# Kernel tuning notes

Hardware: AMD Instinct MI355X
Metric: run time of the kernel (lower is better)

## Reference

```python
import jax, jax.numpy as jnp
import numpy as np

DIM = 100      # number of assets in the basket
M = 50         # time steps
T = 1.0
R = 0.05
SIGMA = 0.2
S0 = 100.0
DT = T / M
H = 128        # hidden_dim of ZetaNetwork
B = 8192       # Monte-Carlo paths (batch)
EPS = 1e-5     # torch LayerNorm eps


def _layernorm(x, g, b):
    mu = jnp.mean(x, axis=-1, keepdims=True)
    var = jnp.mean((x - mu) ** 2, axis=-1, keepdims=True)
    return (x - mu) / jnp.sqrt(var + EPS) * g + b


def setup_inputs() -> dict:
    key = jax.random.key(0)
    ks = jax.random.split(key, 12)
    dw = jax.random.normal(ks[0], (B, M, DIM), dtype=jnp.float32)
    t_grid = jax.random.uniform(ks[1], (B, M), dtype=jnp.float32)
    s = 0.05
    inp = {
        "dw": dw,
        "t_grid": t_grid,
        "W1": jax.random.normal(ks[2], (DIM + 1, H), dtype=jnp.float32) * s,
        "b1": jnp.zeros((H,), jnp.float32),
        "g1": jnp.ones((H,), jnp.float32),
        "be1": jnp.zeros((H,), jnp.float32),
        "W2": jax.random.normal(ks[3], (H, H), dtype=jnp.float32) * s,
        "b2": jnp.zeros((H,), jnp.float32),
        "g2": jnp.ones((H,), jnp.float32),
        "be2": jnp.zeros((H,), jnp.float32),
        "W3": jax.random.normal(ks[4], (H, H), dtype=jnp.float32) * s,
        "b3": jnp.zeros((H,), jnp.float32),
        "g3": jnp.ones((H,), jnp.float32),
        "be3": jnp.zeros((H,), jnp.float32),
        "W4": jax.random.normal(ks[5], (H, DIM), dtype=jnp.float32) * s,
        "b4": jnp.zeros((DIM,), jnp.float32),
        "Y0": jnp.array([10.0], dtype=jnp.float32),
    }
    return inp


def reference(dw, t_grid, W1, b1, g1, be1, W2, b2, g2, be2,
              W3, b3, g3, be3, W4, b4, Y0):
    batch = dw.shape[0]

    def zeta_net(x):  # x: [B, DIM+1]
        h = jax.nn.gelu(_layernorm(x @ W1 + b1, g1, be1), approximate=False)
        h = jax.nn.gelu(_layernorm(h @ W2 + b2, g2, be2), approximate=False)
        h = jax.nn.gelu(_layernorm(h @ W3 + b3, g3, be3), approximate=False)
        return jax.nn.sigmoid(h @ W4 + b4)  # [B, DIM]

    def step(carry, xs):
        S, Y = carry
        dw_i, t_i = xs                                   # [B,DIM], [B,1]
        net_in = jnp.concatenate([S / S0, t_i], axis=1)  # [B,DIM+1]
        zeta = zeta_net(net_in)
        dS = S * (R * DT + SIGMA * dw_i)
        portfolio_gain = jnp.sum(zeta * dS, axis=1, keepdims=True)
        asset_val = jnp.sum(zeta * S, axis=1, keepdims=True)
        Y = Y + R * (Y - asset_val) * DT + portfolio_gain
        S = S + dS
        return (S, Y), None

    S_init = jnp.full((batch, DIM), S0, dtype=dw.dtype)
    Y_init = jnp.ones((batch, 1), dtype=dw.dtype) * Y0
    xs = (jnp.swapaxes(dw, 0, 1),                # [M,B,DIM]
          jnp.swapaxes(t_grid, 0, 1)[..., None])  # [M,B,1]
    (S, Y), _ = jax.lax.scan(step, (S_init, Y_init), xs)
    return (Y, S)
```

## Files before the change

### kernel.cpp

```cpp
#include <hip/hip_runtime.h>
#include <hip/hip_bf16.h>
#include <cstdint>
#include <cstddef>

typedef __attribute__((ext_vector_type(8))) short short8;
typedef __attribute__((ext_vector_type(4))) float f32x4;
typedef __attribute__((ext_vector_type(4))) unsigned int u32x4;

#define NDIM 100
#define NSTEP 50
#define NPATH 8192
#define XSTR 128
#define ESTR 128

typedef const __attribute__((address_space(1))) unsigned int glb_u32;
typedef __attribute__((address_space(3))) unsigned int lds_u32;

__device__ __forceinline__ unsigned short f2b(float f){
  unsigned int u = __float_as_uint(f);
  u += 0x7fffu + ((u >> 16) & 1u);
  return (unsigned short)(u >> 16);
}
__device__ __forceinline__ float b2f(unsigned short h){
  return __uint_as_float(((unsigned int)h) << 16);
}
__device__ __forceinline__ float gelu_fast(float y){
  float u = __builtin_amdgcn_exp2f(-2.4554673f * y);
  return y * __builtin_amdgcn_rcpf(1.f + u);
}
__device__ __forceinline__ float sigm_fast(float x){
  float u = __builtin_amdgcn_exp2f(-1.4426950f * x);
  return __builtin_amdgcn_rcpf(1.f + u);
}

__global__ __launch_bounds__(256) void prep_weights(
    const float* __restrict__ W1, const float* __restrict__ W2,
    const float* __restrict__ W3, const float* __restrict__ W4,
    unsigned short* __restrict__ WTS)
{
  int idx = blockIdx.x * 256 + threadIdx.x;
  int j = idx & 7;
  int s = (idx >> 3) & 15;
  int n = (idx >> 7) & 127;
  int L = idx >> 14;
  int lc = s ^ (n & 15);
  int k  = j * 16 + lc;
  float v;
  if (L == 0)      v = (k <= NDIM) ? W1[k * 128 + n] : 0.f;
  else if (L == 1) v = W2[k * 128 + n];
  else if (L == 2) v = W3[k * 128 + n];
  else             v = (n < NDIM) ? W4[k * NDIM + n] : 0.f;
  WTS[idx] = f2b(v);
}

__global__ __launch_bounds__(256) void prep_params(
    const float* __restrict__ b1, const float* __restrict__ g1, const float* __restrict__ be1,
    const float* __restrict__ b2, const float* __restrict__ g2, const float* __restrict__ be2,
    const float* __restrict__ b3, const float* __restrict__ g3, const float* __restrict__ be3,
    const float* __restrict__ b4, float* __restrict__ PPAR)
{
  int idx = blockIdx.x * 256 + threadIdx.x;
  if (idx >= 1536) return;
  int ct = idx & 7;
  int c  = (idx >> 3) & 15;
  int p  = (idx >> 7) % 3;
  int L  = idx / 384;
  int col = ct * 16 + c;
  const float* v;
  if (L == 0)      v = (p == 0) ? b1 : (p == 1) ? g1 : be1;
  else if (L == 1) v = (p == 0) ? b2 : (p == 1) ? g2 : be2;
  else if (L == 2) v = (p == 0) ? b3 : (p == 1) ? g3 : be3;
  else             v = b4;
  float val;
  if (L == 3) val = (p == 0 && col < NDIM) ? b4[col] : 0.f;
  else        val = v[col];
  PPAR[idx] = val;
}

__global__ __launch_bounds__(256) void phaseA(
    const float* __restrict__ dw, const float* __restrict__ tg,
    unsigned short* __restrict__ X, unsigned short* __restrict__ E,
    float* __restrict__ Sout, int path0)
{
  const int pb = threadIdx.x >> 6;
  const int t  = threadIdx.x & 63;
  const int bl = blockIdx.x * 4 + pb;
  const int b  = path0 + bl;
  const int d0 = (t & 7) * 16 + (t >> 3);
  const int d1 = d0 + 8;
  float s0 = 100.f, s1 = 100.f;
  const float* dwb = dw + (long)b * NSTEP * NDIM;
  const float* tgb = tg + (long)b * NSTEP;
  unsigned short* Xb = X + (long)bl * NSTEP * XSTR;
  unsigned short* Eb = E + (long)bl * NSTEP * ESTR;
  for (int i = 0; i < NSTEP; ++i){
    float tv = tgb[i];
    float w0 = (d0 < NDIM) ? dwb[i * NDIM + d0] : 0.f;
    float w1 = (d1 < NDIM) ? dwb[i * NDIM + d1] : 0.f;
    unsigned short* Xr = Xb + i * XSTR;
    unsigned short* Er = Eb + i * ESTR;
    Xr[t]      = (d0 < NDIM) ? f2b(s0 * 0.01f) : ((d0 == NDIM) ? f2b(tv) : (unsigned short)0);
    Xr[t + 64] = (d1 < NDIM) ? f2b(s1 * 0.01f) : (unsigned short)0;
    Er[t]      = (d0 < NDIM) ? f2b(0.2f * s0 * w0) : (unsigned short)0;
    Er[t + 64] = (d1 < NDIM) ? f2b(0.2f * s1 * w1) : (unsigned short)0;
    s0 = fmaf(s0, 0.001f + 0.2f * w0, s0);
    s1 = fmaf(s1, 0.001f + 0.2f * w1, s1);
  }
  if (d0 < NDIM) Sout[(long)b * NDIM + d0] = s0;
  if (d1 < NDIM) Sout[(long)b * NDIM + d1] = s1;
}

__global__ __launch_bounds__(256, 3) void phaseB(
    const unsigned short* __restrict__ X,
    const unsigned short* __restrict__ E,
    const unsigned short* __restrict__ WTS,
    const float* __restrict__ PPAR,
    float* __restrict__ cbuf, long row0)
{
  __shared__ __align__(16) char lds[49152];
  char* const wbuf = lds;
  const int tid = threadIdx.x;
  const int w = tid >> 6;
  const int l = tid & 63;
  const int g = l >> 4;
  const int c = l & 15;
  char* const H = lds + 32768 + w * 4096;
  const long base = (long)blockIdx.x * 128 + w * 16;

  auto stage = [&](int Loff){
    #pragma unroll
    for (int it = 0; it < 8; ++it){
      int chunk = w * 8 + it;
      __builtin_amdgcn_global_load_lds((glb_u32*)(WTS + Loff + chunk * 512 + l * 8),
          (lds_u32*)(wbuf + chunk * 1024), 16, 0, 0);
    }
  };

  short8 af0[4], af1[4];
  {
    const unsigned short* xr0 = X + (base + c) * XSTR;
    const unsigned short* xr1 = X + (base + 64 + c) * XSTR;
    #pragma unroll
    for (int ks = 0; ks < 4; ++ks){
      af0[ks] = *(const short8*)(xr0 + 32 * ks + 8 * g);
      af1[ks] = *(const short8*)(xr1 + 32 * ks + 8 * g);
    }
  }

  auto mfma2 = [&](f32x4 (&acc0)[8], f32x4 (&acc1)[8], f32x4 blo, f32x4 bhi){
    #pragma unroll
    for (int ct = 0; ct < 8; ++ct){
      float bs = (ct < 4) ? blo[ct] : bhi[ct - 4];
      f32x4 z; z[0] = bs; z[1] = bs; z[2] = bs; z[3] = bs;
      acc0[ct] = z; acc1[ct] = z;
      const char* rowp = wbuf + ((ct * 16 + c) << 8);
      #pragma unroll
      for (int ks = 0; ks < 4; ++ks){
        short8 bf = *(const short8*)(rowp + (((4 * ks + g) ^ c) << 4));
        acc0[ct] = __builtin_amdgcn_mfma_f32_16x16x32_bf16(af0[ks], bf, acc0[ct], 0, 0, 0);
        acc1[ct] = __builtin_amdgcn_mfma_f32_16x16x32_bf16(af1[ks], bf, acc1[ct], 0, 0, 0);
      }
    }
  };

  auto postproc = [&](f32x4 (&acc)[8], short8 (&af)[4],
                      f32x4 glo, f32x4 ghi, f32x4 belo, f32x4 behi){
    #pragma unroll
    for (int j = 0; j < 4; ++j){
      float s1 = 0.f, s2 = 0.f;
      #pragma unroll
      for (int ct = 0; ct < 8; ++ct){ float x = acc[ct][j]; s1 += x; s2 = fmaf(x, x, s2); }
      s1 += __shfl_xor(s1, 1, 64); s2 += __shfl_xor(s2, 1, 64);
      s1 += __shfl_xor(s1, 2, 64); s2 += __shfl_xor(s2, 2, 64);
      s1 += __shfl_xor(s1, 4, 64); s2 += __shfl_xor(s2, 4, 64);
      s1 += __shfl_xor(s1, 8, 64); s2 += __shfl_xor(s2, 8, 64);
      float mu = s1 * 0.0078125f;
      float rstd = rsqrtf(fmaf(-mu, mu, s2 * 0.0078125f) + 1e-5f);
      int row = 4 * g + j;
      u32x4 ov;
      #pragma unroll
      for (int p = 0; p < 4; ++p){
        float ga  = (p < 2) ? glo[2*p]     : ghi[2*p - 4];
        float gb  = (p < 2) ? glo[2*p + 1] : ghi[2*p - 3];
        float ba  = (p < 2) ? belo[2*p]     : behi[2*p - 4];
        float bb2 = (p < 2) ? belo[2*p + 1] : behi[2*p - 3];
        float A0 = rstd * ga, A1 = rstd * gb;
        float C0 = fmaf(-mu, A0, ba), C1 = fmaf(-mu, A1, bb2);
        float h0 = gelu_fast(fmaf(acc[2*p    ][j], A0, C0));
        float h1 = gelu_fast(fmaf(acc[2*p + 1][j], A1, C1));
        unsigned int pk;
        asm("v_cvt_pk_bf16_f32 %0, %1, %2" : "=v"(pk) : "v"(h0), "v"(h1));
        ov[p] = pk;
      }
      *(u32x4*)(H + row * 256 + ((c ^ row) << 4)) = ov;
    }
    #pragma unroll
    for (int ks = 0; ks < 4; ++ks)
      af[ks] = *(const short8*)(H + c * 256 + (((4 * ks + g) ^ c) << 4));
  };

  auto epilogue = [&](f32x4 (&acc)[8], short8 (&ep)[4], long rbase){
    #pragma unroll
    for (int j = 0; j < 4; ++j){
      float pg = 0.f;
      #pragma unroll
      for (int ct = 0; ct < 8; ++ct){
        float z = sigm_fast(acc[ct][j]);
        pg = fmaf(z, b2f((unsigned short)ep[j][ct]), pg);
      }
      pg += __shfl_xor(pg, 1, 64);
      pg += __shfl_xor(pg, 2, 64);
      pg += __shfl_xor(pg, 4, 64);
      pg += __shfl_xor(pg, 8, 64);
      if (c == 0) cbuf[row0 + rbase + 4 * g + j] = pg;
    }
  };

  stage(0);
  __syncthreads();

  #pragma unroll
  for (int L = 0; L < 3; ++L){
    const float* pp = PPAR + L * 384 + c * 8;
    f32x4 blo  = *(const f32x4*)pp,         bhi  = *(const f32x4*)(pp + 4);
    f32x4 glo  = *(const f32x4*)(pp + 128), ghi  = *(const f32x4*)(pp + 132);
    f32x4 belo = *(const f32x4*)(pp + 256), behi = *(const f32x4*)(pp + 260);
    f32x4 acc0[8], acc1[8];
    mfma2(acc0, acc1, blo, bhi);
    __syncthreads();
    stage((L + 1) * 16384);
    postproc(acc0, af0, glo, ghi, belo, behi);
    postproc(acc1, af1, glo, ghi, belo, behi);
    __syncthreads();
  }

  {
    const float* pp = PPAR + 3 * 384 + c * 8;
    f32x4 blo = *(const f32x4*)pp, bhi = *(const f32x4*)(pp + 4);
    short8 ep0[4], ep1[4];
    #pragma unroll
    for (int j = 0; j < 4; ++j){
      ep0[j] = *(const short8*)(E + (base + 4 * g + j) * ESTR + c * 8);
      ep1[j] = *(const short8*)(E + (base + 64 + 4 * g + j) * ESTR + c * 8);
    }
    f32x4 acc0[8], acc1[8];
    mfma2(acc0, acc1, blo, bhi);
    epilogue(acc0, ep0, base);
    epilogue(acc1, ep1, base + 64);
  }
}

__global__ __launch_bounds__(256) void phaseC(const float* __restrict__ cbuf,
                                              const float* __restrict__ Y0,
                                              float* __restrict__ Yout)
{
  int b = blockIdx.x * 256 + threadIdx.x;
  if (b >= NPATH) return;
  const float kk = 1.0f + 0.05f * (1.0f / 50.0f);
  float y = Y0[0];
  const float* cb = cbuf + (long)b * NSTEP;
  #pragma unroll 10
  for (int i = 0; i < NSTEP; ++i) y = y * kk + cb[i];
  Yout[b] = y;
}

extern "C" void kernel_launch(void* const* d_in, const int* in_sizes, int n_in,
                              void* d_out, int out_size, void* d_ws, size_t ws_size,
                              hipStream_t stream)
{
  const float* dw  = (const float*)d_in[0];
  const float* tg  = (const float*)d_in[1];
  const float* W1  = (const float*)d_in[2];
  const float* b1  = (const float*)d_in[3];
  const float* g1  = (const float*)d_in[4];
  const float* be1 = (const float*)d_in[5];
  const float* W2  = (const float*)d_in[6];
  const float* b2  = (const float*)d_in[7];
  const float* g2  = (const float*)d_in[8];
  const float* be2 = (const float*)d_in[9];
  const float* W3  = (const float*)d_in[10];
  const float* b3  = (const float*)d_in[11];
  const float* g3  = (const float*)d_in[12];
  const float* be3 = (const float*)d_in[13];
  const float* W4  = (const float*)d_in[14];
  const float* b4  = (const float*)d_in[15];
  const float* Y0  = (const float*)d_in[16];
  float* out = (float*)d_out;

  char* ws = (char*)d_ws;
  unsigned short* WTS = (unsigned short*)ws;
  float* PPAR = (float*)(ws + 131072);
  float* cbuf = (float*)(ws + 137344);
  char* chunk = ws + 1775744;

  prep_weights<<<256, 256, 0, stream>>>(W1, W2, W3, W4, WTS);
  prep_params<<<6, 256, 0, stream>>>(b1, g1, be1, b2, g2, be2, b3, g3, be3, b4, PPAR);

  long avail = (long)ws_size - 1775744L;
  long pc = (avail > 0) ? (avail / 25600L) : 0;
  if (pc > 8192) pc = 8192;
  pc -= pc % 128;
  if (pc < 128) pc = 128;

  for (long p0 = 0; p0 < 8192; p0 += pc){
    long np = 8192 - p0; if (np > pc) np = pc;
    unsigned short* Xc = (unsigned short*)chunk;
    unsigned short* Ec = Xc + np * 50L * XSTR;
    phaseA<<<(int)(np / 4), 256, 0, stream>>>(dw, tg, Xc, Ec, out + 8192, (int)p0);
    long nrows = np * 50L;
    phaseB<<<(int)(nrows / 128), 256, 0, stream>>>(Xc, Ec, WTS, PPAR, cbuf, p0 * 50L);
  }
  phaseC<<<32, 256, 0, stream>>>(cbuf, Y0, out);
}
```

Before: 215.5 us.

## Double phaseB block to 512 threads and pack LayerNorm/GELU math into float2

phaseB now runs 8 waves per block covering 256 rows instead of 128. Each 32KB weight stage into LDS is therefore shared by twice as many rows, and staging work per wave is halved. The LayerNorm statistics, GELU and sigmoid epilogue are rewritten over float2 pairs so the compiler can emit packed FP32 instructions, and the gamma/beta loads are moved after the MFMA block. LDS per block grows to 64KB, which limits how many blocks fit per CU and may change latency hiding.

```diff
diff --git a/kernel.cpp b/kernel.cpp
--- a/kernel.cpp
+++ b/kernel.cpp
@@ -5,6 +5,7 @@
 
 typedef __attribute__((ext_vector_type(8))) short short8;
 typedef __attribute__((ext_vector_type(4))) float f32x4;
+typedef __attribute__((ext_vector_type(2))) float f32x2;
 typedef __attribute__((ext_vector_type(4))) unsigned int u32x4;
 
 #define NDIM 100
@@ -23,14 +24,6 @@
 }
 __device__ __forceinline__ float b2f(unsigned short h){
   return __uint_as_float(((unsigned int)h) << 16);
-}
-__device__ __forceinline__ float gelu_fast(float y){
-  float u = __builtin_amdgcn_exp2f(-2.4554673f * y);
-  return y * __builtin_amdgcn_rcpf(1.f + u);
-}
-__device__ __forceinline__ float sigm_fast(float x){
-  float u = __builtin_amdgcn_exp2f(-1.4426950f * x);
-  return __builtin_amdgcn_rcpf(1.f + u);
 }
 
 __global__ __launch_bounds__(256) void prep_weights(
@@ -110,14 +103,14 @@
   if (d1 < NDIM) Sout[(long)b * NDIM + d1] = s1;
 }
 
-__global__ __launch_bounds__(256, 3) void phaseB(
+__global__ __launch_bounds__(512, 4) void phaseB(
     const unsigned short* __restrict__ X,
     const unsigned short* __restrict__ E,
     const unsigned short* __restrict__ WTS,
     const float* __restrict__ PPAR,
     float* __restrict__ cbuf, long row0)
 {
-  __shared__ __align__(16) char lds[49152];
+  __shared__ __align__(16) char lds[65536];
   char* const wbuf = lds;
   const int tid = threadIdx.x;
   const int w = tid >> 6;
@@ -125,12 +118,12 @@
   const int g = l >> 4;
   const int c = l & 15;
   char* const H = lds + 32768 + w * 4096;
-  const long base = (long)blockIdx.x * 128 + w * 16;
+  const long base = (long)blockIdx.x * 256 + w * 16;
 
   auto stage = [&](int Loff){
     #pragma unroll
-    for (int it = 0; it < 8; ++it){
-      int chunk = w * 8 + it;
+    for (int it = 0; it < 4; ++it){
+      int chunk = it * 8 + w;
       __builtin_amdgcn_global_load_lds((glb_u32*)(WTS + Loff + chunk * 512 + l * 8),
           (lds_u32*)(wbuf + chunk * 1024), 16, 0, 0);
     }
@@ -139,7 +132,7 @@
   short8 af0[4], af1[4];
   {
     const unsigned short* xr0 = X + (base + c) * XSTR;
-    const unsigned short* xr1 = X + (base + 64 + c) * XSTR;
+    const unsigned short* xr1 = X + (base + 128 + c) * XSTR;
     #pragma unroll
     for (int ks = 0; ks < 4; ++ks){
       af0[ks] = *(const short8*)(xr0 + 32 * ks + 8 * g);
@@ -163,56 +156,106 @@
     }
   };
 
+  auto gelu2 = [&](f32x2 y) -> f32x2 {
+    f32x2 a = y * -2.4554673f;
+    f32x2 u;
+    u[0] = __builtin_amdgcn_exp2f(a[0]);
+    u[1] = __builtin_amdgcn_exp2f(a[1]);
+    f32x2 d = u + 1.0f;
+    f32x2 r;
+    r[0] = __builtin_amdgcn_rcpf(d[0]);
+    r[1] = __builtin_amdgcn_rcpf(d[1]);
+    return y * r;
+  };
+
   auto postproc = [&](f32x4 (&acc)[8], short8 (&af)[4],
                       f32x4 glo, f32x4 ghi, f32x4 belo, f32x4 behi){
-    #pragma unroll
-    for (int j = 0; j < 4; ++j){
-      float s1 = 0.f, s2 = 0.f;
-      #pragma unroll
-      for (int ct = 0; ct < 8; ++ct){ float x = acc[ct][j]; s1 += x; s2 = fmaf(x, x, s2); }
-      s1 += __shfl_xor(s1, 1, 64); s2 += __shfl_xor(s2, 1, 64);
-      s1 += __shfl_xor(s1, 2, 64); s2 += __shfl_xor(s2, 2, 64);
-      s1 += __shfl_xor(s1, 4, 64); s2 += __shfl_xor(s2, 4, 64);
-      s1 += __shfl_xor(s1, 8, 64); s2 += __shfl_xor(s2, 8, 64);
-      float mu = s1 * 0.0078125f;
-      float rstd = rsqrtf(fmaf(-mu, mu, s2 * 0.0078125f) + 1e-5f);
-      int row = 4 * g + j;
-      u32x4 ov;
-      #pragma unroll
-      for (int p = 0; p < 4; ++p){
-        float ga  = (p < 2) ? glo[2*p]     : ghi[2*p - 4];
-        float gb  = (p < 2) ? glo[2*p + 1] : ghi[2*p - 3];
-        float ba  = (p < 2) ? belo[2*p]     : behi[2*p - 4];
-        float bb2 = (p < 2) ? belo[2*p + 1] : behi[2*p - 3];
-        float A0 = rstd * ga, A1 = rstd * gb;
-        float C0 = fmaf(-mu, A0, ba), C1 = fmaf(-mu, A1, bb2);
-        float h0 = gelu_fast(fmaf(acc[2*p    ][j], A0, C0));
-        float h1 = gelu_fast(fmaf(acc[2*p + 1][j], A1, C1));
-        unsigned int pk;
-        asm("v_cvt_pk_bf16_f32 %0, %1, %2" : "=v"(pk) : "v"(h0), "v"(h1));
-        ov[p] = pk;
-      }
-      *(u32x4*)(H + row * 256 + ((c ^ row) << 4)) = ov;
-    }
+    f32x2 sA = {0.f, 0.f}, sB = {0.f, 0.f}, qA = {0.f, 0.f}, qB = {0.f, 0.f};
+    #pragma unroll
+    for (int ct = 0; ct < 8; ++ct){
+      f32x2 xy = __builtin_shufflevector(acc[ct], acc[ct], 0, 1);
+      f32x2 zw = __builtin_shufflevector(acc[ct], acc[ct], 2, 3);
+      sA += xy; qA += xy * xy;
+      sB += zw; qB += zw * zw;
+    }
+    #pragma unroll
+    for (int m = 1; m <= 8; m <<= 1){
+      f32x2 t;
+      t[0] = __shfl_xor(sA[0], m, 64); t[1] = __shfl_xor(sA[1], m, 64); sA += t;
+      t[0] = __shfl_xor(sB[0], m, 64); t[1] = __shfl_xor(sB[1], m, 64); sB += t;
+      t[0] = __shfl_xor(qA[0], m, 64); t[1] = __shfl_xor(qA[1], m, 64); qA += t;
+      t[0] = __shfl_xor(qB[0], m, 64); t[1] = __shfl_xor(qB[1], m, 64); qB += t;
+    }
+    f32x2 muA = sA * 0.0078125f, muB = sB * 0.0078125f;
+    f32x2 vA = qA * 0.0078125f - muA * muA + 1e-5f;
+    f32x2 vB = qB * 0.0078125f - muB * muB + 1e-5f;
+    f32x2 rA, rB;
+    rA[0] = rsqrtf(vA[0]); rA[1] = rsqrtf(vA[1]);
+    rB[0] = rsqrtf(vB[0]); rB[1] = rsqrtf(vB[1]);
+    u32x4 ov0, ov1, ov2, ov3;
+    #pragma unroll
+    for (int p = 0; p < 4; ++p){
+      float ga0 = (p < 2) ? glo[2*p]     : ghi[2*p - 4];
+      float ga1 = (p < 2) ? glo[2*p + 1] : ghi[2*p - 3];
+      float be0 = (p < 2) ? belo[2*p]     : behi[2*p - 4];
+      float be1 = (p < 2) ? belo[2*p + 1] : behi[2*p - 3];
+      f32x2 xyE = __builtin_shufflevector(acc[2*p],   acc[2*p],   0, 1);
+      f32x2 zwE = __builtin_shufflevector(acc[2*p],   acc[2*p],   2, 3);
+      f32x2 xyO = __builtin_shufflevector(acc[2*p+1], acc[2*p+1], 0, 1);
+      f32x2 zwO = __builtin_shufflevector(acc[2*p+1], acc[2*p+1], 2, 3);
+      f32x2 AEA = rA * ga0, AEB = rB * ga0;
+      f32x2 AOA = rA * ga1, AOB = rB * ga1;
+      f32x2 hEA = gelu2(xyE * AEA + (be0 - muA * AEA));
+      f32x2 hEB = gelu2(zwE * AEB + (be0 - muB * AEB));
+      f32x2 hOA = gelu2(xyO * AOA + (be1 - muA * AOA));
+      f32x2 hOB = gelu2(zwO * AOB + (be1 - muB * AOB));
+      unsigned int k0, k1, k2, k3;
+      asm("v_cvt_pk_bf16_f32 %0, %1, %2" : "=v"(k0) : "v"(hEA[0]), "v"(hOA[0]));
+      asm("v_cvt_pk_bf16_f32 %0, %1, %2" : "=v"(k1) : "v"(hEA[1]), "v"(hOA[1]));
+      asm("v_cvt_pk_bf16_f32 %0, %1, %2" : "=v"(k2) : "v"(hEB[0]), "v"(hOB[0]));
+      asm("v_cvt_pk_bf16_f32 %0, %1, %2" : "=v"(k3) : "v"(hEB[1]), "v"(hOB[1]));
+      ov0[p] = k0; ov1[p] = k1; ov2[p] = k2; ov3[p] = k3;
+    }
+    int r0 = 4 * g;
+    *(u32x4*)(H + (r0 + 0) * 256 + ((c ^ (r0 + 0)) << 4)) = ov0;
+    *(u32x4*)(H + (r0 + 1) * 256 + ((c ^ (r0 + 1)) << 4)) = ov1;
+    *(u32x4*)(H + (r0 + 2) * 256 + ((c ^ (r0 + 2)) << 4)) = ov2;
+    *(u32x4*)(H + (r0 + 3) * 256 + ((c ^ (r0 + 3)) << 4)) = ov3;
     #pragma unroll
     for (int ks = 0; ks < 4; ++ks)
       af[ks] = *(const short8*)(H + c * 256 + (((4 * ks + g) ^ c) << 4));
   };
 
   auto epilogue = [&](f32x4 (&acc)[8], short8 (&ep)[4], long rbase){
-    #pragma unroll
-    for (int j = 0; j < 4; ++j){
-      float pg = 0.f;
-      #pragma unroll
-      for (int ct = 0; ct < 8; ++ct){
-        float z = sigm_fast(acc[ct][j]);
-        pg = fmaf(z, b2f((unsigned short)ep[j][ct]), pg);
-      }
-      pg += __shfl_xor(pg, 1, 64);
-      pg += __shfl_xor(pg, 2, 64);
-      pg += __shfl_xor(pg, 4, 64);
-      pg += __shfl_xor(pg, 8, 64);
-      if (c == 0) cbuf[row0 + rbase + 4 * g + j] = pg;
+    f32x2 pgA = {0.f, 0.f}, pgB = {0.f, 0.f};
+    #pragma unroll
+    for (int ct = 0; ct < 8; ++ct){
+      f32x2 xy = __builtin_shufflevector(acc[ct], acc[ct], 0, 1);
+      f32x2 zw = __builtin_shufflevector(acc[ct], acc[ct], 2, 3);
+      f32x2 aA = xy * -1.4426950f, aB = zw * -1.4426950f;
+      f32x2 u, d, r;
+      u[0] = __builtin_amdgcn_exp2f(aA[0]); u[1] = __builtin_amdgcn_exp2f(aA[1]);
+      d = u + 1.f;
+      r[0] = __builtin_amdgcn_rcpf(d[0]); r[1] = __builtin_amdgcn_rcpf(d[1]);
+      f32x2 eA = { b2f((unsigned short)ep[0][ct]), b2f((unsigned short)ep[1][ct]) };
+      pgA += r * eA;
+      u[0] = __builtin_amdgcn_exp2f(aB[0]); u[1] = __builtin_amdgcn_exp2f(aB[1]);
+      d = u + 1.f;
+      r[0] = __builtin_amdgcn_rcpf(d[0]); r[1] = __builtin_amdgcn_rcpf(d[1]);
+      f32x2 eB = { b2f((unsigned short)ep[2][ct]), b2f((unsigned short)ep[3][ct]) };
+      pgB += r * eB;
+    }
+    #pragma unroll
+    for (int m = 1; m <= 8; m <<= 1){
+      f32x2 t;
+      t[0] = __shfl_xor(pgA[0], m, 64); t[1] = __shfl_xor(pgA[1], m, 64); pgA += t;
+      t[0] = __shfl_xor(pgB[0], m, 64); t[1] = __shfl_xor(pgB[1], m, 64); pgB += t;
+    }
+    if (c == 0){
+      cbuf[row0 + rbase + 4 * g + 0] = pgA[0];
+      cbuf[row0 + rbase + 4 * g + 1] = pgA[1];
+      cbuf[row0 + rbase + 4 * g + 2] = pgB[0];
+      cbuf[row0 + rbase + 4 * g + 3] = pgB[1];
     }
   };
 
@@ -222,11 +265,11 @@
   #pragma unroll
   for (int L = 0; L < 3; ++L){
     const float* pp = PPAR + L * 384 + c * 8;
-    f32x4 blo  = *(const f32x4*)pp,         bhi  = *(const f32x4*)(pp + 4);
+    f32x4 blo = *(const f32x4*)pp, bhi = *(const f32x4*)(pp + 4);
+    f32x4 acc0[8], acc1[8];
+    mfma2(acc0, acc1, blo, bhi);
     f32x4 glo  = *(const f32x4*)(pp + 128), ghi  = *(const f32x4*)(pp + 132);
     f32x4 belo = *(const f32x4*)(pp + 256), behi = *(const f32x4*)(pp + 260);
-    f32x4 acc0[8], acc1[8];
-    mfma2(acc0, acc1, blo, bhi);
     __syncthreads();
     stage((L + 1) * 16384);
     postproc(acc0, af0, glo, ghi, belo, behi);
@@ -241,12 +284,12 @@
     #pragma unroll
     for (int j = 0; j < 4; ++j){
       ep0[j] = *(const short8*)(E + (base + 4 * g + j) * ESTR + c * 8);
-      ep1[j] = *(const short8*)(E + (base + 64 + 4 * g + j) * ESTR + c * 8);
+      ep1[j] = *(const short8*)(E + (base + 128 + 4 * g + j) * ESTR + c * 8);
     }
     f32x4 acc0[8], acc1[8];
     mfma2(acc0, acc1, blo, bhi);
     epilogue(acc0, ep0, base);
-    epilogue(acc1, ep1, base + 64);
+    epilogue(acc1, ep1, base + 128);
   }
 }
 
@@ -308,7 +351,7 @@
     unsigned short* Ec = Xc + np * 50L * XSTR;
     phaseA<<<(int)(np / 4), 256, 0, stream>>>(dw, tg, Xc, Ec, out + 8192, (int)p0);
     long nrows = np * 50L;
-    phaseB<<<(int)(nrows / 128), 256, 0, stream>>>(Xc, Ec, WTS, PPAR, cbuf, p0 * 50L);
+    phaseB<<<(int)(nrows / 256), 512, 0, stream>>>(Xc, Ec, WTS, PPAR, cbuf, p0 * 50L);
   }
   phaseC<<<32, 256, 0, stream>>>(cbuf, Y0, out);
 }
```

Result: slower. 236.3 us (+9.7%).

## Fuse path simulation and MLP kernels into one software-pipelined launch

Applied to the files above, without the earlier changes.

Merges phaseA (path simulation writing bf16 X/E) and phaseB (MLP on MFMA) into one kernel whose grid dispatches simulation blocks for chunk k alongside MLP blocks for chunk k-1. Double-buffered chunk storage and a smaller chunk size cap (1024 paths) let the memory-bound simulation overlap the compute-bound MLP. It also moves the gamma/beta loads after the first MFMA batch. This costs extra launches (9 instead of 1 pair) and a shared launch-bounds/LDS footprint for the light phaseA blocks.

```diff
diff --git a/kernel.cpp b/kernel.cpp
--- a/kernel.cpp
+++ b/kernel.cpp
@@ -77,47 +77,49 @@
   PPAR[idx] = val;
 }
 
-__global__ __launch_bounds__(256) void phaseA(
+__global__ __launch_bounds__(256, 3) void fusedAB(
     const float* __restrict__ dw, const float* __restrict__ tg,
-    unsigned short* __restrict__ X, unsigned short* __restrict__ E,
-    float* __restrict__ Sout, int path0)
-{
-  const int pb = threadIdx.x >> 6;
-  const int t  = threadIdx.x & 63;
-  const int bl = blockIdx.x * 4 + pb;
-  const int b  = path0 + bl;
-  const int d0 = (t & 7) * 16 + (t >> 3);
-  const int d1 = d0 + 8;
-  float s0 = 100.f, s1 = 100.f;
-  const float* dwb = dw + (long)b * NSTEP * NDIM;
-  const float* tgb = tg + (long)b * NSTEP;
-  unsigned short* Xb = X + (long)bl * NSTEP * XSTR;
-  unsigned short* Eb = E + (long)bl * NSTEP * ESTR;
-  for (int i = 0; i < NSTEP; ++i){
-    float tv = tgb[i];
-    float w0 = (d0 < NDIM) ? dwb[i * NDIM + d0] : 0.f;
-    float w1 = (d1 < NDIM) ? dwb[i * NDIM + d1] : 0.f;
-    unsigned short* Xr = Xb + i * XSTR;
-    unsigned short* Er = Eb + i * ESTR;
-    Xr[t]      = (d0 < NDIM) ? f2b(s0 * 0.01f) : ((d0 == NDIM) ? f2b(tv) : (unsigned short)0);
-    Xr[t + 64] = (d1 < NDIM) ? f2b(s1 * 0.01f) : (unsigned short)0;
-    Er[t]      = (d0 < NDIM) ? f2b(0.2f * s0 * w0) : (unsigned short)0;
-    Er[t + 64] = (d1 < NDIM) ? f2b(0.2f * s1 * w1) : (unsigned short)0;
-    s0 = fmaf(s0, 0.001f + 0.2f * w0, s0);
-    s1 = fmaf(s1, 0.001f + 0.2f * w1, s1);
-  }
-  if (d0 < NDIM) Sout[(long)b * NDIM + d0] = s0;
-  if (d1 < NDIM) Sout[(long)b * NDIM + d1] = s1;
-}
-
-__global__ __launch_bounds__(256, 3) void phaseB(
-    const unsigned short* __restrict__ X,
-    const unsigned short* __restrict__ E,
+    unsigned short* __restrict__ XA, unsigned short* __restrict__ EA,
+    float* __restrict__ Sout, int path0A, int nA,
+    const unsigned short* __restrict__ XB,
+    const unsigned short* __restrict__ EB,
     const unsigned short* __restrict__ WTS,
     const float* __restrict__ PPAR,
-    float* __restrict__ cbuf, long row0)
+    float* __restrict__ cbuf, long row0B)
 {
   __shared__ __align__(16) char lds[49152];
+
+  if ((int)blockIdx.x < nA){
+    const int pb = threadIdx.x >> 6;
+    const int t  = threadIdx.x & 63;
+    const int bl = blockIdx.x * 4 + pb;
+    const int b  = path0A + bl;
+    const int d0 = (t & 7) * 16 + (t >> 3);
+    const int d1 = d0 + 8;
+    float s0 = 100.f, s1 = 100.f;
+    const float* dwb = dw + (long)b * NSTEP * NDIM;
+    const float* tgb = tg + (long)b * NSTEP;
+    unsigned short* Xb_ = XA + (long)bl * NSTEP * XSTR;
+    unsigned short* Eb_ = EA + (long)bl * NSTEP * ESTR;
+    for (int i = 0; i < NSTEP; ++i){
+      float tv = tgb[i];
+      float w0 = (d0 < NDIM) ? dwb[i * NDIM + d0] : 0.f;
+      float w1 = (d1 < NDIM) ? dwb[i * NDIM + d1] : 0.f;
+      unsigned short* Xr = Xb_ + i * XSTR;
+      unsigned short* Er = Eb_ + i * ESTR;
+      Xr[t]      = (d0 < NDIM) ? f2b(s0 * 0.01f) : ((d0 == NDIM) ? f2b(tv) : (unsigned short)0);
+      Xr[t + 64] = (d1 < NDIM) ? f2b(s1 * 0.01f) : (unsigned short)0;
+      Er[t]      = (d0 < NDIM) ? f2b(0.2f * s0 * w0) : (unsigned short)0;
+      Er[t + 64] = (d1 < NDIM) ? f2b(0.2f * s1 * w1) : (unsigned short)0;
+      s0 = fmaf(s0, 0.001f + 0.2f * w0, s0);
+      s1 = fmaf(s1, 0.001f + 0.2f * w1, s1);
+    }
+    if (d0 < NDIM) Sout[(long)b * NDIM + d0] = s0;
+    if (d1 < NDIM) Sout[(long)b * NDIM + d1] = s1;
+    return;
+  }
+
+  const int bid = blockIdx.x - nA;
   char* const wbuf = lds;
   const int tid = threadIdx.x;
   const int w = tid >> 6;
@@ -125,7 +127,7 @@
   const int g = l >> 4;
   const int c = l & 15;
   char* const H = lds + 32768 + w * 4096;
-  const long base = (long)blockIdx.x * 128 + w * 16;
+  const long base = (long)bid * 128 + w * 16;
 
   auto stage = [&](int Loff){
     #pragma unroll
@@ -138,8 +140,8 @@
 
   short8 af0[4], af1[4];
   {
-    const unsigned short* xr0 = X + (base + c) * XSTR;
-    const unsigned short* xr1 = X + (base + 64 + c) * XSTR;
+    const unsigned short* xr0 = XB + (base + c) * XSTR;
+    const unsigned short* xr1 = XB + (base + 64 + c) * XSTR;
     #pragma unroll
     for (int ks = 0; ks < 4; ++ks){
       af0[ks] = *(const short8*)(xr0 + 32 * ks + 8 * g);
@@ -212,7 +214,7 @@
       pg += __shfl_xor(pg, 2, 64);
       pg += __shfl_xor(pg, 4, 64);
       pg += __shfl_xor(pg, 8, 64);
-      if (c == 0) cbuf[row0 + rbase + 4 * g + j] = pg;
+      if (c == 0) cbuf[row0B + rbase + 4 * g + j] = pg;
     }
   };
 
@@ -223,10 +225,10 @@
   for (int L = 0; L < 3; ++L){
     const float* pp = PPAR + L * 384 + c * 8;
     f32x4 blo  = *(const f32x4*)pp,         bhi  = *(const f32x4*)(pp + 4);
+    f32x4 acc0[8], acc1[8];
+    mfma2(acc0, acc1, blo, bhi);
     f32x4 glo  = *(const f32x4*)(pp + 128), ghi  = *(const f32x4*)(pp + 132);
     f32x4 belo = *(const f32x4*)(pp + 256), behi = *(const f32x4*)(pp + 260);
-    f32x4 acc0[8], acc1[8];
-    mfma2(acc0, acc1, blo, bhi);
     __syncthreads();
     stage((L + 1) * 16384);
     postproc(acc0, af0, glo, ghi, belo, behi);
@@ -240,8 +242,8 @@
     short8 ep0[4], ep1[4];
     #pragma unroll
     for (int j = 0; j < 4; ++j){
-      ep0[j] = *(const short8*)(E + (base + 4 * g + j) * ESTR + c * 8);
-      ep1[j] = *(const short8*)(E + (base + 64 + 4 * g + j) * ESTR + c * 8);
+      ep0[j] = *(const short8*)(EB + (base + 4 * g + j) * ESTR + c * 8);
+      ep1[j] = *(const short8*)(EB + (base + 64 + 4 * g + j) * ESTR + c * 8);
     }
     f32x4 acc0[8], acc1[8];
     mfma2(acc0, acc1, blo, bhi);
@@ -291,24 +293,40 @@
   unsigned short* WTS = (unsigned short*)ws;
   float* PPAR = (float*)(ws + 131072);
   float* cbuf = (float*)(ws + 137344);
-  char* chunk = ws + 1775744;
+  char* chunk0 = ws + 1775744;
 
   prep_weights<<<256, 256, 0, stream>>>(W1, W2, W3, W4, WTS);
   prep_params<<<6, 256, 0, stream>>>(b1, g1, be1, b2, g2, be2, b3, g3, be3, b4, PPAR);
 
   long avail = (long)ws_size - 1775744L;
-  long pc = (avail > 0) ? (avail / 25600L) : 0;
-  if (pc > 8192) pc = 8192;
+  long pc = (avail > 0) ? (avail / 51200L) : 0;
+  if (pc > 1024) pc = 1024;
   pc -= pc % 128;
   if (pc < 128) pc = 128;
 
-  for (long p0 = 0; p0 < 8192; p0 += pc){
+  long prev_p0 = 0, prev_np = 0;
+  int k = 0;
+  for (long p0 = 0; p0 < 8192; p0 += pc, ++k){
     long np = 8192 - p0; if (np > pc) np = pc;
-    unsigned short* Xc = (unsigned short*)chunk;
-    unsigned short* Ec = Xc + np * 50L * XSTR;
-    phaseA<<<(int)(np / 4), 256, 0, stream>>>(dw, tg, Xc, Ec, out + 8192, (int)p0);
-    long nrows = np * 50L;
-    phaseB<<<(int)(nrows / 128), 256, 0, stream>>>(Xc, Ec, WTS, PPAR, cbuf, p0 * 50L);
+    unsigned short* Xa = (unsigned short*)(chunk0 + (long)(k & 1) * pc * 25600L);
+    unsigned short* Ea = Xa + pc * 50L * XSTR;
+    int nA = (int)(np / 4);
+    int nB = (int)(prev_np * 50L / 128L);
+    const unsigned short* Xb_ = nullptr;
+    const unsigned short* Eb_ = nullptr;
+    if (nB > 0){
+      const unsigned short* Xp = (const unsigned short*)(chunk0 + (long)((k - 1) & 1) * pc * 25600L);
+      Xb_ = Xp; Eb_ = Xp + pc * 50L * XSTR;
+    }
+    fusedAB<<<nA + nB, 256, 0, stream>>>(dw, tg, Xa, Ea, out + 8192, (int)p0, nA,
+        Xb_, Eb_, WTS, PPAR, cbuf, prev_p0 * 50L);
+    prev_p0 = p0; prev_np = np;
+  }
+  {
+    int nB = (int)(prev_np * 50L / 128L);
+    const unsigned short* Xp = (const unsigned short*)(chunk0 + (long)((k - 1) & 1) * pc * 25600L);
+    fusedAB<<<nB, 256, 0, stream>>>(dw, tg, nullptr, nullptr, out + 8192, 0, 0,
+        Xp, Xp + pc * 50L * XSTR, WTS, PPAR, cbuf, prev_p0 * 50L);
   }
   phaseC<<<32, 256, 0, stream>>>(cbuf, Y0, out);
 }
```

New measurement: 270.3 us. 25.4% more time.
